# Kernel tuning notes

Hardware: AMD Instinct MI355X
Metric: run time of the kernel (lower is better)

## Reference

```python
import jax, jax.numpy as jnp
import numpy as np

B = 128      # batch
L = 28       # seq len (MNIST rows)
F = 28       # input feature (MNIST cols)
DM = 256     # d_model
EXPAND = 2
DI = EXPAND * DM   # d_inner = 512
DS = 16      # d_state
DR = DM // 16      # dt_rank = 16
K = 3        # d_conv
NL = 5       # n_layers
OUT = 10     # output_size


def setup_inputs() -> dict:
    key = jax.random.key(0)
    ks = jax.random.split(key, 12)
    s = 0.02
    x = jax.random.normal(ks[0], (B, 1, L, F), jnp.float32)
    input_proj_w = jax.random.normal(ks[1], (DM, F), jnp.float32) * s
    in_proj_w = jax.random.normal(ks[2], (NL, 2 * DI, DM), jnp.float32) * s
    conv_w = jax.random.normal(ks[3], (NL, DI, K), jnp.float32) * s
    conv_b = jnp.zeros((NL, DI), jnp.float32)
    x_proj_w = jax.random.normal(ks[4], (NL, DR + 2 * DS, DI), jnp.float32) * s
    dt_proj_w = jax.random.normal(ks[5], (NL, DI, DR), jnp.float32) * s
    dt_proj_b = jnp.full((NL, DI), -4.0, jnp.float32)  # softplus -> small dt
    # S4D-real init: A = -[1..d_state]
    A_log = jnp.log(jnp.broadcast_to(jnp.arange(1, DS + 1, dtype=jnp.float32), (NL, DI, DS)))
    D = jnp.ones((NL, DI), jnp.float32)
    out_proj_w = jax.random.normal(ks[6], (NL, DM, DI), jnp.float32) * s
    classifier_w = jax.random.normal(ks[7], (OUT, DM), jnp.float32) * s
    return {"x": x, "input_proj_w": input_proj_w, "in_proj_w": in_proj_w,
            "conv_w": conv_w, "conv_b": conv_b, "x_proj_w": x_proj_w,
            "dt_proj_w": dt_proj_w, "dt_proj_b": dt_proj_b, "A_log": A_log,
            "D": D, "out_proj_w": out_proj_w, "classifier_w": classifier_w}


def mamba_block(h, in_w, cw, cb, xw, dtw, dtb, A_log, D_vec, ow):
    # h: (B, L, DM)
    xz = h @ in_w.T                      # (B, L, 2*DI)
    xb, z = jnp.split(xz, 2, axis=-1)    # each (B, L, DI)
    # causal depthwise conv over time
    xc = xb.transpose(0, 2, 1)           # (B, DI, L)
    xc = jax.lax.conv_general_dilated(
        xc, cw[:, None, :], window_strides=(1,), padding=[(K - 1, 0)],
        dimension_numbers=("NCH", "OIH", "NCH"), feature_group_count=DI)
    xc = xc + cb[None, :, None]
    u = jax.nn.silu(xc.transpose(0, 2, 1))          # (B, L, DI)
    dbc = u @ xw.T                                   # (B, L, DR+2*DS)
    dt, Bm, Cm = dbc[..., :DR], dbc[..., DR:DR + DS], dbc[..., DR + DS:]
    delta = jax.nn.softplus(dt @ dtw.T + dtb)        # (B, L, DI)
    A = -jnp.exp(A_log)                              # (DI, DS)

    def step(hst, t):
        u_t, d_t, b_t, c_t = t                       # (B,DI),(B,DI),(B,DS),(B,DS)
        hst = jnp.exp(d_t[..., None] * A) * hst + (d_t * u_t)[..., None] * b_t[:, None, :]
        y = jnp.einsum("bds,bs->bd", hst, c_t)
        return hst, y

    h0 = jnp.zeros((u.shape[0], DI, DS), u.dtype)
    xs = (u.transpose(1, 0, 2), delta.transpose(1, 0, 2),
          Bm.transpose(1, 0, 2), Cm.transpose(1, 0, 2))
    _, ys = jax.lax.scan(step, h0, xs)               # (L, B, DI)
    y = ys.transpose(1, 0, 2) + u * D_vec            # skip term D*u
    y = y * jax.nn.silu(z)
    return y @ ow.T                                  # (B, L, DM)


def reference(x, input_proj_w, in_proj_w, conv_w, conv_b, x_proj_w,
              dt_proj_w, dt_proj_b, A_log, D, out_proj_w, classifier_w):
    h = x[:, 0] @ input_proj_w.T                     # squeeze(1), (B, L, DM)
    for i in range(NL):
        h = h + mamba_block(h, in_proj_w[i], conv_w[i], conv_b[i], x_proj_w[i],
                            dt_proj_w[i], dt_proj_b[i], A_log[i], D[i], out_proj_w[i])
    pooled = h.mean(axis=1)                          # (B, DM)
    return pooled @ classifier_w.T                   # (B, OUT)
```

## Files before the change

kernel.cpp:

```cpp
#include <hip/hip_runtime.h>
#include <hip/hip_bf16.h>
#include <cstdint>

#define BB 128
#define LL 28
#define FF 28
#define DM 256
#define DI 512
#define DS 16
#define DR 16
#define KK 3
#define NLAYER 5
#define NOUT 10
#define NTOK (BB * LL)
#define NDBC (DR + 2 * DS)

#define N_INW (NLAYER * 2 * DI * DM)
#define N_OPW (NLAYER * DM * DI)
#define N_XPW (NLAYER * NDBC * DI)

typedef __attribute__((ext_vector_type(8))) short bf16x8;
typedef __attribute__((ext_vector_type(4))) float f32x4;

__device__ __forceinline__ float sigmoidf_(float x) { return 1.0f / (1.0f + __expf(-x)); }
__device__ __forceinline__ float siluf_(float x) { return x * sigmoidf_(x); }
__device__ __forceinline__ float softplus_fast(float x) {
    return (x > 20.0f) ? x : __logf(1.0f + __expf(x));
}

__global__ void cast_weights(const float* __restrict__ inw, const float* __restrict__ opw,
                             const float* __restrict__ xpw,
                             __hip_bfloat16* __restrict__ inwb, __hip_bfloat16* __restrict__ opwb,
                             __hip_bfloat16* __restrict__ xpwb) {
    int i = (blockIdx.x * 256 + threadIdx.x) * 4;
    const float* s; __hip_bfloat16* d; int off;
    if (i < N_INW) { s = inw; d = inwb; off = i; }
    else if (i < N_INW + N_OPW) { s = opw; d = opwb; off = i - N_INW; }
    else if (i < N_INW + N_OPW + N_XPW) { s = xpw; d = xpwb; off = i - N_INW - N_OPW; }
    else return;
    float4 v = *(const float4*)&s[off];
    d[off + 0] = __float2bfloat16(v.x);
    d[off + 1] = __float2bfloat16(v.y);
    d[off + 2] = __float2bfloat16(v.z);
    d[off + 3] = __float2bfloat16(v.w);
}

__global__ __launch_bounds__(256) void g_inputproj_f32(
        const float* __restrict__ A, const float* __restrict__ W,
        float* __restrict__ C, __hip_bfloat16* __restrict__ Cb) {
    constexpr int BM = 64, BN = 64, K = FF, N = DM;
    __shared__ float As[16][BM + 4];
    __shared__ float Ws[16][BN + 4];
    const int tid = threadIdx.x;
    const int kk = tid & 15, row = tid >> 4;
    const int tx = tid & 15, ty = tid >> 4;
    const int bm = blockIdx.y * BM, bn = blockIdx.x * BN;
    float acc[4][4];
    #pragma unroll
    for (int i = 0; i < 4; ++i)
        #pragma unroll
        for (int j = 0; j < 4; ++j) acc[i][j] = 0.f;
    for (int k0 = 0; k0 < K; k0 += 16) {
        const int k = k0 + kk;
        const bool kok = (k < K);
        #pragma unroll
        for (int r = 0; r < 4; ++r) {
            As[kk][r * 16 + row] = kok ? A[(size_t)(bm + r * 16 + row) * K + k] : 0.f;
            Ws[kk][r * 16 + row] = kok ? W[(size_t)(bn + r * 16 + row) * K + k] : 0.f;
        }
        __syncthreads();
        #pragma unroll
        for (int k2 = 0; k2 < 16; ++k2) {
            float a[4], b[4];
            #pragma unroll
            for (int i = 0; i < 4; ++i) a[i] = As[k2][ty * 4 + i];
            #pragma unroll
            for (int j = 0; j < 4; ++j) b[j] = Ws[k2][tx * 4 + j];
            #pragma unroll
            for (int i = 0; i < 4; ++i)
                #pragma unroll
                for (int j = 0; j < 4; ++j) acc[i][j] += a[i] * b[j];
        }
        __syncthreads();
    }
    #pragma unroll
    for (int i = 0; i < 4; ++i) {
        const int m = bm + ty * 4 + i;
        #pragma unroll
        for (int j = 0; j < 4; ++j) {
            const int n = bn + tx * 4 + j;
            float v = acc[i][j];
            C[(size_t)m * N + n] = v;
            Cb[(size_t)m * N + n] = __float2bfloat16(v);
        }
    }
}

__global__ __launch_bounds__(256) void k_xz_conv(
        const __hip_bfloat16* __restrict__ hb,
        const __hip_bfloat16* __restrict__ inw_l,
        const float* __restrict__ convw_l,
        const float* __restrict__ convb_l,
        __hip_bfloat16* __restrict__ ub,
        __hip_bfloat16* __restrict__ gzb) {
    __shared__ __align__(16) __hip_bfloat16 As[32][264];
    __shared__ __align__(16) __hip_bfloat16 Ws[64][264];
    __shared__ __align__(16) __hip_bfloat16 xbt[32][72];

    const int b = blockIdx.y;
    const int n0 = blockIdx.x * 64;
    const int t = threadIdx.x;
    const int wave = t >> 6, lane = t & 63;
    const int rla = lane & 15, koff = (lane >> 4) * 8;
    const int lrow = (lane >> 4) * 4, lcol = lane & 15;

    for (int i = t; i < 28 * 32; i += 256) {
        const int r = i >> 5, c = (i & 31) * 8;
        *(int4*)&As[r][c] = *(const int4*)&hb[(size_t)(b * LL + r) * DM + c];
    }
    for (int i = t; i < 64 * 32; i += 256) {
        const int r = i >> 5, c = (i & 31) * 8;
        *(int4*)&Ws[r][c] = *(const int4*)&inw_l[(size_t)(n0 + r) * DM + c];
    }
    __syncthreads();

    f32x4 acc0 = {}, acc1 = {};
    #pragma unroll
    for (int ks = 0; ks < 8; ++ks) {
        bf16x8 bf = *(const bf16x8*)&Ws[wave * 16 + rla][ks * 32 + koff];
        bf16x8 a0 = *(const bf16x8*)&As[rla][ks * 32 + koff];
        bf16x8 a1 = *(const bf16x8*)&As[16 + rla][ks * 32 + koff];
        acc0 = __builtin_amdgcn_mfma_f32_16x16x32_bf16(a0, bf, acc0, 0, 0, 0);
        acc1 = __builtin_amdgcn_mfma_f32_16x16x32_bf16(a1, bf, acc1, 0, 0, 0);
    }

    const int ncol = wave * 16 + lcol;
    if (n0 < DI) {
        #pragma unroll
        for (int r = 0; r < 4; ++r) {
            const int m0 = lrow + r, m1 = 16 + lrow + r;
            xbt[m0][ncol] = __float2bfloat16(acc0[r]);
            if (m1 < LL) xbt[m1][ncol] = __float2bfloat16(acc1[r]);
        }
        __syncthreads();
        const int col = t & 63, lg = t >> 6;
        const int di = n0 + col;
        const float c0 = convw_l[di * KK + 0];
        const float c1 = convw_l[di * KK + 1];
        const float c2 = convw_l[di * KK + 2];
        const float cbv = convb_l[di];
        const int l0 = lg * 7;
        float xm2 = (l0 >= 2) ? __bfloat162float(xbt[l0 - 2][col]) : 0.f;
        float xm1 = (l0 >= 1) ? __bfloat162float(xbt[l0 - 1][col]) : 0.f;
        #pragma unroll
        for (int j = 0; j < 7; ++j) {
            const int l = l0 + j;
            const float x0 = __bfloat162float(xbt[l][col]);
            const float v = siluf_(cbv + c0 * xm2 + c1 * xm1 + c2 * x0);
            xm2 = xm1; xm1 = x0;
            ub[(size_t)(b * LL + l) * DI + di] = __float2bfloat16(v);
        }
    } else {
        const int zc = n0 - DI + ncol;
        #pragma unroll
        for (int r = 0; r < 4; ++r) {
            const int m0 = lrow + r, m1 = 16 + lrow + r;
            gzb[(size_t)(b * LL + m0) * DI + zc] = __float2bfloat16(siluf_(acc0[r]));
            if (m1 < LL)
                gzb[(size_t)(b * LL + m1) * DI + zc] = __float2bfloat16(siluf_(acc1[r]));
        }
    }
}

__global__ __launch_bounds__(256) void k_xproj(
        const __hip_bfloat16* __restrict__ ub,
        const __hip_bfloat16* __restrict__ xpw_l,
        float* __restrict__ dbc) {
    __shared__ __align__(16) __hip_bfloat16 As[32][520];

    const int m0 = blockIdx.x * 32;
    const int t = threadIdx.x;
    const int wave = t >> 6, lane = t & 63;
    const int rla = lane & 15, koff = (lane >> 4) * 8;
    const int lrow = (lane >> 4) * 4, lcol = lane & 15;

    for (int i = t; i < 32 * 64; i += 256) {
        const int r = i >> 6, c = (i & 63) * 8;
        *(int4*)&As[r][c] = *(const int4*)&ub[(size_t)(m0 + r) * DI + c];
    }
    __syncthreads();

    #pragma unroll
    for (int cc = 0; cc < 2; ++cc) {
        const int c = wave + cc * 4;
        if (c < 6) {
            const int mt = c & 1, nt = c >> 1;
            f32x4 acc = {};
            #pragma unroll
            for (int ks = 0; ks < 16; ++ks) {
                bf16x8 bf = *(const bf16x8*)&xpw_l[(size_t)(nt * 16 + rla) * DI + ks * 32 + koff];
                bf16x8 af = *(const bf16x8*)&As[mt * 16 + rla][ks * 32 + koff];
                acc = __builtin_amdgcn_mfma_f32_16x16x32_bf16(af, bf, acc, 0, 0, 0);
            }
            #pragma unroll
            for (int r = 0; r < 4; ++r)
                dbc[(size_t)(m0 + mt * 16 + lrow + r) * NDBC + nt * 16 + lcol] = acc[r];
        }
    }
}

__global__ __launch_bounds__(256) void k_scan(
        const __hip_bfloat16* __restrict__ ub,
        const __hip_bfloat16* __restrict__ gzb,
        const float* __restrict__ dbc,
        const float* __restrict__ dtw_l,
        const float* __restrict__ dtb_l,
        const float* __restrict__ alog_l,
        const float* __restrict__ Dvec_l,
        __hip_bfloat16* __restrict__ yb) {
    __shared__ __align__(16) __hip_bfloat16 sus[LL][64];
    __shared__ __align__(16) __hip_bfloat16 sgz[LL][64];
    __shared__ float sdbc[LL][NDBC];
    __shared__ float sdelta[LL][64];
    __shared__ __align__(16) __hip_bfloat16 sy[LL][64];

    const int b = blockIdx.x;
    const int cg = blockIdx.y;
    const int di0 = cg * 64;
    const int t = threadIdx.x;
    const int wave = t >> 6, lane = t & 63;

    for (int i = t; i < 224; i += 256) {
        const int r = i >> 3, c = (i & 7) * 8;
        *(int4*)&sus[r][c] = *(const int4*)&ub[(size_t)(b * LL + r) * DI + di0 + c];
        *(int4*)&sgz[r][c] = *(const int4*)&gzb[(size_t)(b * LL + r) * DI + di0 + c];
    }
    {
        const float4* s4 = (const float4*)(dbc + (size_t)b * LL * NDBC);
        float4* d4 = (float4*)&sdbc[0][0];
        for (int i = t; i < LL * NDBC / 4; i += 256) d4[i] = s4[i];
    }

    float wrow[DR];
    {
        const float4* w4 = (const float4*)(dtw_l + (size_t)(di0 + lane) * DR);
        #pragma unroll
        for (int q = 0; q < DR / 4; ++q) {
            float4 v = w4[q];
            wrow[q * 4 + 0] = v.x; wrow[q * 4 + 1] = v.y;
            wrow[q * 4 + 2] = v.z; wrow[q * 4 + 3] = v.w;
        }
    }
    const float dbias = dtb_l[di0 + lane];
    __syncthreads();

    #pragma unroll
    for (int j = 0; j < 7; ++j) {
        const int l = wave * 7 + j;
        const float4 q0 = *(const float4*)&sdbc[l][0];
        const float4 q1 = *(const float4*)&sdbc[l][4];
        const float4 q2 = *(const float4*)&sdbc[l][8];
        const float4 q3 = *(const float4*)&sdbc[l][12];
        float d0 = wrow[0] * q0.x + wrow[1] * q0.y + wrow[2] * q0.z + wrow[3] * q0.w;
        float d1 = wrow[4] * q1.x + wrow[5] * q1.y + wrow[6] * q1.z + wrow[7] * q1.w;
        float d2 = wrow[8] * q2.x + wrow[9] * q2.y + wrow[10] * q2.z + wrow[11] * q2.w;
        float d3 = wrow[12] * q3.x + wrow[13] * q3.y + wrow[14] * q3.z + wrow[15] * q3.w;
        sdelta[l][lane] = softplus_fast(((d0 + d1) + (d2 + d3)) + dbias);
    }

    const int c = t >> 2, sq = t & 3;
    const int di = di0 + c;
    float4 aq = *(const float4*)&alog_l[(size_t)di * DS + sq * 4];
    const float A0 = -__expf(aq.x), A1 = -__expf(aq.y);
    const float A2 = -__expf(aq.z), A3 = -__expf(aq.w);
    const float Dd = Dvec_l[di];

    __syncthreads();

    float st0 = 0.f, st1 = 0.f, st2 = 0.f, st3 = 0.f;
    #pragma unroll 2
    for (int l = 0; l < LL; ++l) {
        const float d = sdelta[l][c];
        const float uu = __bfloat162float(sus[l][c]);
        const float du = d * uu;
        const float4 Bq = *(const float4*)&sdbc[l][DR + sq * 4];
        const float4 Cq = *(const float4*)&sdbc[l][DR + DS + sq * 4];
        st0 = __expf(d * A0) * st0 + du * Bq.x;
        st1 = __expf(d * A1) * st1 + du * Bq.y;
        st2 = __expf(d * A2) * st2 + du * Bq.z;
        st3 = __expf(d * A3) * st3 + du * Bq.w;
        float yp = st0 * Cq.x + st1 * Cq.y + st2 * Cq.z + st3 * Cq.w;
        yp += __shfl_xor(yp, 1);
        yp += __shfl_xor(yp, 2);
        if (sq == 0) {
            const float g = __bfloat162float(sgz[l][c]);
            sy[l][c] = __float2bfloat16((yp + uu * Dd) * g);
        }
    }
    __syncthreads();

    for (int i = t; i < 224; i += 256) {
        const int r = i >> 3, cc = (i & 7) * 8;
        *(int4*)&yb[(size_t)(b * LL + r) * DI + di0 + cc] = *(const int4*)&sy[r][cc];
    }
}

__global__ __launch_bounds__(256) void k_outproj(
        const __hip_bfloat16* __restrict__ yb,
        const __hip_bfloat16* __restrict__ opw_l,
        float* __restrict__ h,
        __hip_bfloat16* __restrict__ hb) {
    __shared__ __align__(16) __hip_bfloat16 As[32][520];

    const int b = blockIdx.y;
    const int n0 = blockIdx.x * 32;
    const int t = threadIdx.x;
    const int wave = t >> 6, lane = t & 63;
    const int rla = lane & 15, koff = (lane >> 4) * 8;
    const int lrow = (lane >> 4) * 4, lcol = lane & 15;

    for (int i = t; i < 28 * 64; i += 256) {
        const int r = i >> 6, c = (i & 63) * 8;
        *(int4*)&As[r][c] = *(const int4*)&yb[(size_t)(b * LL + r) * DI + c];
    }
    __syncthreads();

    const int mt = wave & 1, nt = wave >> 1;
    f32x4 acc = {};
    #pragma unroll
    for (int ks = 0; ks < 16; ++ks) {
        bf16x8 bf = *(const bf16x8*)&opw_l[(size_t)(n0 + nt * 16 + rla) * DI + ks * 32 + koff];
        bf16x8 af = *(const bf16x8*)&As[mt * 16 + rla][ks * 32 + koff];
        acc = __builtin_amdgcn_mfma_f32_16x16x32_bf16(af, bf, acc, 0, 0, 0);
    }
    #pragma unroll
    for (int r = 0; r < 4; ++r) {
        const int m = mt * 16 + lrow + r;
        if (m < LL) {
            const int n = n0 + nt * 16 + lcol;
            const size_t idx = (size_t)(b * LL + m) * DM + n;
            const float v = h[idx] + acc[r];
            h[idx] = v;
            hb[idx] = __float2bfloat16(v);
        }
    }
}

__global__ void pool_classifier_kernel(const float* __restrict__ h,
                                       const float* __restrict__ cls,
                                       float* __restrict__ out) {
    const int b = blockIdx.x;
    const int dm = threadIdx.x;
    __shared__ float pool[DM];
    float p = 0.f;
    for (int l = 0; l < LL; ++l) p += h[(size_t)(b * LL + l) * DM + dm];
    pool[dm] = p * (1.0f / LL);
    __syncthreads();
    if (dm < NOUT) {
        float acc = 0.f;
        for (int k = 0; k < DM; ++k) acc += pool[k] * cls[dm * DM + k];
        out[b * NOUT + dm] = acc;
    }
}

extern "C" void kernel_launch(void* const* d_in, const int* in_sizes, int n_in,
                              void* d_out, int out_size, void* d_ws, size_t ws_size,
                              hipStream_t stream) {
    const float* x       = (const float*)d_in[0];
    const float* ipw     = (const float*)d_in[1];
    const float* inw     = (const float*)d_in[2];
    const float* convw   = (const float*)d_in[3];
    const float* convb   = (const float*)d_in[4];
    const float* xpw     = (const float*)d_in[5];
    const float* dtw     = (const float*)d_in[6];
    const float* dtb     = (const float*)d_in[7];
    const float* alog    = (const float*)d_in[8];
    const float* Dvec    = (const float*)d_in[9];
    const float* opw     = (const float*)d_in[10];
    const float* clsw    = (const float*)d_in[11];
    float* out = (float*)d_out;

    float* h   = (float*)d_ws;
    float* dbc = h + (size_t)NTOK * DM;
    __hip_bfloat16* hb   = (__hip_bfloat16*)(dbc + (size_t)NTOK * NDBC);
    __hip_bfloat16* ub   = hb + (size_t)NTOK * DM;
    __hip_bfloat16* gzb  = ub + (size_t)NTOK * DI;
    __hip_bfloat16* yb   = gzb + (size_t)NTOK * DI;
    __hip_bfloat16* inwb = yb + (size_t)NTOK * DI;
    __hip_bfloat16* opwb = inwb + N_INW;
    __hip_bfloat16* xpwb = opwb + N_OPW;

    hipLaunchKernelGGL(cast_weights, dim3((N_INW + N_OPW + N_XPW) / 1024), dim3(256), 0, stream,
                       inw, opw, xpw, inwb, opwb, xpwb);

    hipLaunchKernelGGL(g_inputproj_f32, dim3(DM / 64, NTOK / 64), dim3(256), 0, stream,
                       x, ipw, h, hb);

    for (int layer = 0; layer < NLAYER; ++layer) {
        const __hip_bfloat16* inwb_l = inwb + (size_t)layer * 2 * DI * DM;
        const __hip_bfloat16* xpwb_l = xpwb + (size_t)layer * NDBC * DI;
        const __hip_bfloat16* opwb_l = opwb + (size_t)layer * DM * DI;
        const float* convw_l = convw + (size_t)layer * DI * KK;
        const float* convb_l = convb + (size_t)layer * DI;
        const float* dtw_l   = dtw  + (size_t)layer * DI * DR;
        const float* dtb_l   = dtb  + (size_t)layer * DI;
        const float* alog_l  = alog + (size_t)layer * DI * DS;
        const float* Dvec_l  = Dvec + (size_t)layer * DI;

        hipLaunchKernelGGL(k_xz_conv, dim3(16, BB), dim3(256), 0, stream,
                           hb, inwb_l, convw_l, convb_l, ub, gzb);

        hipLaunchKernelGGL(k_xproj, dim3(NTOK / 32), dim3(256), 0, stream,
                           ub, xpwb_l, dbc);

        hipLaunchKernelGGL(k_scan, dim3(BB, 8), dim3(256), 0, stream,
                           ub, gzb, dbc, dtw_l, dtb_l, alog_l, Dvec_l, yb);

        hipLaunchKernelGGL(k_outproj, dim3(8, BB), dim3(256), 0, stream,
                           yb, opwb_l, h, hb);
    }

    hipLaunchKernelGGL(pool_classifier_kernel, dim3(BB), dim3(DM), 0, stream,
                       h, clsw, out);
}
```

Before: 281.5 us.

## Replace LDS-staged xproj and outproj GEMMs with single-wave direct-load MFMA tiles

Rewrites the x_proj and out_proj GEMM kernels so each 64-thread block computes one 16x16 output tile, loading A fragments straight from global memory instead of staging the activation rows in shared memory behind a barrier. This removes the LDS copy and syncthreads and launches many more small blocks to raise parallelism. In exchange, activation rows are re-read from global/L2 by every column tile rather than shared, and the out_proj padding rows are clamped to a valid address.

After: 299.4 us. 6.4% more time.

```diff
diff --git a/kernel.cpp b/kernel.cpp
--- a/kernel.cpp
+++ b/kernel.cpp
@@ -172,41 +172,26 @@
     }
 }
 
-__global__ __launch_bounds__(256) void k_xproj(
+__global__ __launch_bounds__(64) void k_xproj_ns(
         const __hip_bfloat16* __restrict__ ub,
         const __hip_bfloat16* __restrict__ xpw_l,
         float* __restrict__ dbc) {
-    __shared__ __align__(16) __hip_bfloat16 As[32][520];
-
-    const int m0 = blockIdx.x * 32;
-    const int t = threadIdx.x;
-    const int wave = t >> 6, lane = t & 63;
+    const int m0 = blockIdx.x * 16;
+    const int nt = blockIdx.y;
+    const int lane = threadIdx.x;
     const int rla = lane & 15, koff = (lane >> 4) * 8;
     const int lrow = (lane >> 4) * 4, lcol = lane & 15;
 
-    for (int i = t; i < 32 * 64; i += 256) {
-        const int r = i >> 6, c = (i & 63) * 8;
-        *(int4*)&As[r][c] = *(const int4*)&ub[(size_t)(m0 + r) * DI + c];
-    }
-    __syncthreads();
-
-    #pragma unroll
-    for (int cc = 0; cc < 2; ++cc) {
-        const int c = wave + cc * 4;
-        if (c < 6) {
-            const int mt = c & 1, nt = c >> 1;
-            f32x4 acc = {};
-            #pragma unroll
-            for (int ks = 0; ks < 16; ++ks) {
-                bf16x8 bf = *(const bf16x8*)&xpw_l[(size_t)(nt * 16 + rla) * DI + ks * 32 + koff];
-                bf16x8 af = *(const bf16x8*)&As[mt * 16 + rla][ks * 32 + koff];
-                acc = __builtin_amdgcn_mfma_f32_16x16x32_bf16(af, bf, acc, 0, 0, 0);
-            }
-            #pragma unroll
-            for (int r = 0; r < 4; ++r)
-                dbc[(size_t)(m0 + mt * 16 + lrow + r) * NDBC + nt * 16 + lcol] = acc[r];
-        }
-    }
+    f32x4 acc = {};
+    #pragma unroll
+    for (int ks = 0; ks < 16; ++ks) {
+        bf16x8 af = *(const bf16x8*)&ub[(size_t)(m0 + rla) * DI + ks * 32 + koff];
+        bf16x8 bf = *(const bf16x8*)&xpw_l[(size_t)(nt * 16 + rla) * DI + ks * 32 + koff];
+        acc = __builtin_amdgcn_mfma_f32_16x16x32_bf16(af, bf, acc, 0, 0, 0);
+    }
+    #pragma unroll
+    for (int r = 0; r < 4; ++r)
+        dbc[(size_t)(m0 + lrow + r) * NDBC + nt * 16 + lcol] = acc[r];
 }
 
 __global__ __launch_bounds__(256) void k_scan(
@@ -305,40 +290,33 @@
     }
 }
 
-__global__ __launch_bounds__(256) void k_outproj(
+__global__ __launch_bounds__(64) void k_outproj_ns(
         const __hip_bfloat16* __restrict__ yb,
         const __hip_bfloat16* __restrict__ opw_l,
         float* __restrict__ h,
         __hip_bfloat16* __restrict__ hb) {
-    __shared__ __align__(16) __hip_bfloat16 As[32][520];
-
     const int b = blockIdx.y;
-    const int n0 = blockIdx.x * 32;
-    const int t = threadIdx.x;
-    const int wave = t >> 6, lane = t & 63;
+    const int mt = blockIdx.x & 1;
+    const int nt = blockIdx.x >> 1;
+    const int lane = threadIdx.x;
     const int rla = lane & 15, koff = (lane >> 4) * 8;
     const int lrow = (lane >> 4) * 4, lcol = lane & 15;
 
-    for (int i = t; i < 28 * 64; i += 256) {
-        const int r = i >> 6, c = (i & 63) * 8;
-        *(int4*)&As[r][c] = *(const int4*)&yb[(size_t)(b * LL + r) * DI + c];
-    }
-    __syncthreads();
-
-    const int mt = wave & 1, nt = wave >> 1;
+    int arow = b * LL + mt * 16 + rla;
+    if (arow > NTOK - 1) arow = NTOK - 1;
+
     f32x4 acc = {};
     #pragma unroll
     for (int ks = 0; ks < 16; ++ks) {
-        bf16x8 bf = *(const bf16x8*)&opw_l[(size_t)(n0 + nt * 16 + rla) * DI + ks * 32 + koff];
-        bf16x8 af = *(const bf16x8*)&As[mt * 16 + rla][ks * 32 + koff];
+        bf16x8 af = *(const bf16x8*)&yb[(size_t)arow * DI + ks * 32 + koff];
+        bf16x8 bf = *(const bf16x8*)&opw_l[(size_t)(nt * 16 + rla) * DI + ks * 32 + koff];
         acc = __builtin_amdgcn_mfma_f32_16x16x32_bf16(af, bf, acc, 0, 0, 0);
     }
     #pragma unroll
     for (int r = 0; r < 4; ++r) {
         const int m = mt * 16 + lrow + r;
         if (m < LL) {
-            const int n = n0 + nt * 16 + lcol;
-            const size_t idx = (size_t)(b * LL + m) * DM + n;
+            const size_t idx = (size_t)(b * LL + m) * DM + nt * 16 + lcol;
             const float v = h[idx] + acc[r];
             h[idx] = v;
             hb[idx] = __float2bfloat16(v);
@@ -410,13 +388,13 @@
         hipLaunchKernelGGL(k_xz_conv, dim3(16, BB), dim3(256), 0, stream,
                            hb, inwb_l, convw_l, convb_l, ub, gzb);
 
-        hipLaunchKernelGGL(k_xproj, dim3(NTOK / 32), dim3(256), 0, stream,
+        hipLaunchKernelGGL(k_xproj_ns, dim3(NTOK / 16, 3), dim3(64), 0, stream,
                            ub, xpwb_l, dbc);
 
         hipLaunchKernelGGL(k_scan, dim3(BB, 8), dim3(256), 0, stream,
                            ub, gzb, dbc, dtw_l, dtb_l, alog_l, Dvec_l, yb);
 
-        hipLaunchKernelGGL(k_outproj, dim3(8, BB), dim3(256), 0, stream,
+        hipLaunchKernelGGL(k_outproj_ns, dim3(32, BB), dim3(64), 0, stream,
                            yb, opwb_l, h, hb);
     }
 
```
